# Optimization experiments

Hardware: AMD Instinct MI355X
Metric: run time of the kernel (lower is better)

## Reference

```python
import jax, jax.numpy as jnp
import numpy as np

K_HOPS = 10  # truncation order of the heat-kernel Taylor series


def setup_inputs() -> dict:
    key = jax.random.key(0)
    k1, k2, k3 = jax.random.split(key, 3)
    N, E, D_IN, D_OUT = 50000, 625000, 128, 128
    x = jax.random.normal(k1, (N, D_IN), dtype=jnp.float32)
    edge_index = jax.random.randint(k2, (2, E), 0, N, dtype=jnp.int64)
    t = jnp.asarray(5.0, dtype=jnp.float32)  # learnable diffusion time
    lim = 1.0 / np.sqrt(D_IN)
    W = jax.random.uniform(k3, (D_OUT, D_IN), dtype=jnp.float32, minval=-lim, maxval=lim)
    b = jnp.zeros((D_OUT,), dtype=jnp.float32)
    return {"x": x, "edge_index": edge_index, "t": t, "W": W, "b": b}


def reference(x, edge_index, t, W, b):
    N = x.shape[0]
    loop = jnp.arange(N, dtype=edge_index.dtype)
    src = jnp.concatenate([edge_index[0], loop])  # gcn_norm adds self-loops
    dst = jnp.concatenate([edge_index[1], loop])
    # symmetric normalization: norm_e = deg(dst)^-1/2 * deg(src)^-1/2
    deg = jnp.zeros((N,), dtype=x.dtype).at[dst].add(1.0)
    dinv = jnp.where(deg > 0, jax.lax.rsqrt(deg), 0.0)
    norm = dinv[src] * dinv[dst]  # [E+N]

    def prop(h):  # one hop of A_hat @ h via gather-scale-scatter
        msg = h[src] * norm[:, None]          # [E+N, D]
        return jax.ops.segment_sum(msg, dst, num_segments=N)

    # heat kernel: e^{-t} * sum_k t^k/k! * A_hat^k x
    coeff = jnp.exp(-t)
    out = coeff * x
    h = x
    for k in range(1, K_HOPS + 1):
        h = prop(h)
        coeff = coeff * t / k
        out = out + coeff * h
    return out @ W.T + b
```

## Files before the change

### kernel.cpp

```cpp
#include <hip/hip_runtime.h>
#include <math.h>

typedef float f4 __attribute__((ext_vector_type(4)));
typedef _Float16 h4 __attribute__((ext_vector_type(4)));


__global__ void k_count(const int* __restrict__ dst, int* __restrict__ cnt, int E) {
  int e = blockIdx.x * blockDim.x + threadIdx.x;
  if (e < E) atomicAdd(&cnt[dst[e]], 1);
}

__global__ void k_scan_partial(const int* __restrict__ cnt, int* __restrict__ rowptr,
                               int* __restrict__ bsums, float* __restrict__ dinv, int N) {
  __shared__ int s[1024];
  int tid = threadIdx.x;
  int idx = blockIdx.x * 1024 + tid;
  int v = (idx < N) ? cnt[idx] : 0;
  if (idx < N) dinv[idx] = rsqrtf((float)(v + 1));
  s[tid] = v;
  __syncthreads();
  for (int off = 1; off < 1024; off <<= 1) {
    int add = (tid >= off) ? s[tid - off] : 0;
    __syncthreads();
    s[tid] += add;
    __syncthreads();
  }
  if (idx <= N) rowptr[idx] = s[tid] - v;
  if (tid == 1023) bsums[blockIdx.x] = s[1023];
}

__global__ void k_scan_sums(int* __restrict__ bsums, int nb) {
  __shared__ int s[1024];
  int tid = threadIdx.x;
  int v = (tid < nb) ? bsums[tid] : 0;
  s[tid] = v;
  __syncthreads();
  for (int off = 1; off < 1024; off <<= 1) {
    int add = (tid >= off) ? s[tid - off] : 0;
    __syncthreads();
    s[tid] += add;
    __syncthreads();
  }
  if (tid < nb) bsums[tid] = s[tid] - v;
}

__global__ void k_add_offsets(int* __restrict__ rowptr, int* __restrict__ cursor,
                              const int* __restrict__ bsums, int N) {
  int idx = blockIdx.x * 1024 + threadIdx.x;
  if (idx <= N) {
    int v = rowptr[idx] + bsums[blockIdx.x];
    rowptr[idx] = v;
    if (idx < N) cursor[idx] = v;
  }
}

__global__ void k_scatter(const int* __restrict__ src, const int* __restrict__ dst,
                          const float* __restrict__ dinv, int* __restrict__ cursor,
                          int2* __restrict__ colw, int E) {
  int e = blockIdx.x * blockDim.x + threadIdx.x;
  if (e < E) {
    int s = src[e];
    int d = dst[e];
    int slot = atomicAdd(&cursor[d], 1);
    colw[slot] = make_int2(s, __float_as_int(dinv[s] * dinv[d]));
  }
}

__global__ void k_tohalf(const float* __restrict__ x, _Float16* __restrict__ xh, int total4) {
  int i = blockIdx.x * blockDim.x + threadIdx.x;
  if (i < total4) ((h4*)xh)[i] = __builtin_convertvector(((const f4*)x)[i], h4);
}

__global__ __launch_bounds__(256) void k_hop(
    const int* __restrict__ rowptr, const int2* __restrict__ colw,
    const float* __restrict__ dinv, const h4* __restrict__ xh,
    const h4* __restrict__ yin, h4* __restrict__ yout,
    const float* __restrict__ t_ptr, int j, int first, int N) {
  int wave = threadIdx.x >> 6;
  int lane = threadIdx.x & 63;
  int half = lane >> 5;
  int fl = lane & 31;
  int r = (blockIdx.x * 4 + wave) * 2 + half;
  if (r >= N) return;
  float t = t_ptr[0];
  float cj = expf(-t);
  for (int i = 1; i <= j; ++i) cj *= t / (float)i;
  float gs = first ? cj * t / (float)(j + 1) : 1.0f;

  auto G = [&](int idx) -> f4 {
    return __builtin_convertvector(yin[(size_t)idx * 32 + fl], f4);
  };

  f4 sA = {0,0,0,0}, sB = {0,0,0,0}, sC = {0,0,0,0}, sD = {0,0,0,0};
  int e = rowptr[r], end = rowptr[r + 1];
  for (; e + 3 < end; e += 4) {
    int2 c0 = colw[e], c1 = colw[e + 1], c2 = colw[e + 2], c3 = colw[e + 3];
    sA += __int_as_float(c0.y) * G(c0.x);
    sB += __int_as_float(c1.y) * G(c1.x);
    sC += __int_as_float(c2.y) * G(c2.x);
    sD += __int_as_float(c3.y) * G(c3.x);
  }
  for (; e < end; ++e) {
    int2 c0 = colw[e];
    sA += __int_as_float(c0.y) * G(c0.x);
  }
  f4 s = (sA + sB) + (sC + sD);
  float di = dinv[r];
  s += (di * di) * G(r);
  f4 xr = __builtin_convertvector(xh[(size_t)r * 32 + fl], f4);
  s = gs * s + cj * xr;
  yout[(size_t)r * 32 + fl] = __builtin_convertvector(s, h4);
}

__global__ __launch_bounds__(256) void k_matmul(
    const h4* __restrict__ y16, const float* __restrict__ W,
    const float* __restrict__ bias, float* __restrict__ out, int N) {
  __shared__ float aS[64 * 128];
  __shared__ float wS[64 * 128];
  int tid = threadIdx.x;
  int rbase = blockIdx.x * 64;
  int cbase = blockIdx.y * 64;

  {
    int kq = tid & 31, rr = tid >> 5;
#pragma unroll
    for (int p = 0; p < 8; ++p) {
      int r = p * 8 + rr;
      int gr = rbase + r; if (gr >= N) gr = N - 1;
      f4 va = __builtin_convertvector(y16[(size_t)gr * 32 + kq], f4);
      *(f4*)&aS[r * 128 + ((kq ^ (r & 7)) << 2)] = va;
      f4 vw = *(const f4*)&W[(size_t)(cbase + r) * 128 + kq * 4];
      *(f4*)&wS[r * 128 + ((kq ^ (r & 7)) << 2)] = vw;
    }
  }
  __syncthreads();

  int rg = tid & 15, cg = tid >> 4;
  int sa = rg & 7;
  float s[4][4];
#pragma unroll
  for (int i = 0; i < 4; ++i)
#pragma unroll
    for (int j = 0; j < 4; ++j) s[i][j] = 0.f;

#pragma unroll 4
  for (int kq = 0; kq < 32; ++kq) {
    f4 a4[4], w4[4];
#pragma unroll
    for (int i = 0; i < 4; ++i)
      a4[i] = *(const f4*)&aS[(rg + 16 * i) * 128 + ((kq ^ sa) << 2)];
#pragma unroll
    for (int j = 0; j < 4; ++j) {
      int c = 4 * cg + j;
      w4[j] = *(const f4*)&wS[c * 128 + ((kq ^ (c & 7)) << 2)];
    }
#pragma unroll
    for (int i = 0; i < 4; ++i)
#pragma unroll
      for (int j = 0; j < 4; ++j)
        s[i][j] += a4[i].x * w4[j].x + a4[i].y * w4[j].y +
                   a4[i].z * w4[j].z + a4[i].w * w4[j].w;
  }

  f4 bv = *(const f4*)&bias[cbase + 4 * cg];
#pragma unroll
  for (int i = 0; i < 4; ++i) {
    int r = rbase + rg + 16 * i;
    if (r < N) {
      f4 o;
      o.x = s[i][0] + bv.x; o.y = s[i][1] + bv.y;
      o.z = s[i][2] + bv.z; o.w = s[i][3] + bv.w;
      *(f4*)&out[(size_t)r * 128 + cbase + 4 * cg] = o;
    }
  }
}


extern "C" void kernel_launch(void* const* d_in, const int* in_sizes, int n_in,
                              void* d_out, int out_size, void* d_ws, size_t ws_size,
                              hipStream_t stream) {
  const float* x = (const float*)d_in[0];
  const int* ei = (const int*)d_in[1];
  const float* t = (const float*)d_in[2];
  const float* W = (const float*)d_in[3];
  const float* b = (const float*)d_in[4];
  int N = in_sizes[0] / 128;
  int E = in_sizes[1] / 2;
  const int* srcp = ei;
  const int* dstp = ei + E;
  float* out = (float*)d_out;

  char* ws = (char*)d_ws;
  size_t off = 0;
  auto alloc = [&](size_t bytes) -> void* {
    void* p = ws + off;
    off += (bytes + 255) & ~(size_t)255;
    return p;
  };
  h4*    yh0    = (h4*)alloc((size_t)N * 128 * 2);
  h4*    yh1    = (h4*)alloc((size_t)N * 128 * 2);
  h4*    xh     = (h4*)alloc((size_t)N * 128 * 2);
  int*   cnt    = (int*)alloc((size_t)N * 4);
  float* dinv   = (float*)alloc((size_t)N * 4);
  int*   rowptr = (int*)alloc((size_t)(N + 1) * 4);
  int*   cursor = (int*)alloc((size_t)N * 4);
  int*   bsums  = (int*)alloc(4096);
  int2*  colw   = (int2*)alloc((size_t)E * 8);
  (void)ws_size;

  int nb_scan = (N + 1 + 1023) / 1024;

  hipMemsetAsync(cnt, 0, (size_t)N * 4, stream);
  k_count<<<(E + 255) / 256, 256, 0, stream>>>(dstp, cnt, E);
  k_scan_partial<<<nb_scan, 1024, 0, stream>>>(cnt, rowptr, bsums, dinv, N);
  k_scan_sums<<<1, 1024, 0, stream>>>(bsums, nb_scan);
  k_add_offsets<<<nb_scan, 1024, 0, stream>>>(rowptr, cursor, bsums, N);
  k_scatter<<<(E + 255) / 256, 256, 0, stream>>>(srcp, dstp, dinv, cursor, colw, E);
  k_tohalf<<<(N * 32 + 255) / 256, 256, 0, stream>>>(x, (_Float16*)xh, N * 32);

  int nblk = (N + 7) / 8;
  const h4* yin = xh;
  h4* bufs[2] = {yh0, yh1};
  for (int m = 0; m < 10; ++m) {
    h4* yout = bufs[m & 1];
    k_hop<<<nblk, 256, 0, stream>>>(rowptr, colw, dinv, xh, yin, yout,
                                    t, 9 - m, (m == 0) ? 1 : 0, N);
    yin = yout;
  }

  dim3 mmg((N + 63) / 64, 2);
  k_matmul<<<mmg, 256, 0, stream>>>(yin, W, b, out, N);
}
```

Before: 493.6 us.

## Use 16-byte fp16 gathers in hops and MFMA split-precision final matmul

The hop kernel now gives each row 16 lanes that each load 8 halves (16 bytes), so one wave covers four rows instead of two and each gather uses wider memory transactions. The final projection moves from an FP32 scalar LDS tile matmul to MFMA 16x16x32 f16 instructions. W is split into hi and lo fp16 parts so the fp16 rounding error of the weights is mostly recovered. This should cut matmul time and hop gather overhead, at the cost of fp16 products on activations and uncoalesced scalar output stores.

```diff
diff --git a/kernel.cpp b/kernel.cpp
--- a/kernel.cpp
+++ b/kernel.cpp
@@ -2,7 +2,8 @@
 #include <math.h>
 
 typedef float f4 __attribute__((ext_vector_type(4)));
-typedef _Float16 h4 __attribute__((ext_vector_type(4)));
+typedef float f8 __attribute__((ext_vector_type(8)));
+typedef _Float16 h8 __attribute__((ext_vector_type(8)));
 
 
 __global__ void k_count(const int* __restrict__ dst, int* __restrict__ cnt, int E) {
@@ -66,32 +67,36 @@
   }
 }
 
-__global__ void k_tohalf(const float* __restrict__ x, _Float16* __restrict__ xh, int total4) {
+__global__ void k_tohalf(const float* __restrict__ x, _Float16* __restrict__ xh, int total8) {
   int i = blockIdx.x * blockDim.x + threadIdx.x;
-  if (i < total4) ((h4*)xh)[i] = __builtin_convertvector(((const f4*)x)[i], h4);
+  if (i < total8) {
+    f4 a = ((const f4*)x)[i * 2], b = ((const f4*)x)[i * 2 + 1];
+    f8 v = {a.x, a.y, a.z, a.w, b.x, b.y, b.z, b.w};
+    ((h8*)xh)[i] = __builtin_convertvector(v, h8);
+  }
 }
 
 __global__ __launch_bounds__(256) void k_hop(
     const int* __restrict__ rowptr, const int2* __restrict__ colw,
-    const float* __restrict__ dinv, const h4* __restrict__ xh,
-    const h4* __restrict__ yin, h4* __restrict__ yout,
+    const float* __restrict__ dinv, const h8* __restrict__ xh,
+    const h8* __restrict__ yin, h8* __restrict__ yout,
     const float* __restrict__ t_ptr, int j, int first, int N) {
   int wave = threadIdx.x >> 6;
   int lane = threadIdx.x & 63;
-  int half = lane >> 5;
-  int fl = lane & 31;
-  int r = (blockIdx.x * 4 + wave) * 2 + half;
+  int quarter = lane >> 4;
+  int fl = lane & 15;
+  int r = (blockIdx.x * 4 + wave) * 4 + quarter;
   if (r >= N) return;
   float t = t_ptr[0];
   float cj = expf(-t);
   for (int i = 1; i <= j; ++i) cj *= t / (float)i;
   float gs = first ? cj * t / (float)(j + 1) : 1.0f;
 
-  auto G = [&](int idx) -> f4 {
-    return __builtin_convertvector(yin[(size_t)idx * 32 + fl], f4);
+  auto G = [&](int idx) -> f8 {
+    return __builtin_convertvector(yin[(size_t)idx * 16 + fl], f8);
   };
 
-  f4 sA = {0,0,0,0}, sB = {0,0,0,0}, sC = {0,0,0,0}, sD = {0,0,0,0};
+  f8 sA = {0,0,0,0,0,0,0,0}, sB = sA, sC = sA, sD = sA;
   int e = rowptr[r], end = rowptr[r + 1];
   for (; e + 3 < end; e += 4) {
     int2 c0 = colw[e], c1 = colw[e + 1], c2 = colw[e + 2], c3 = colw[e + 3];
@@ -104,73 +109,80 @@
     int2 c0 = colw[e];
     sA += __int_as_float(c0.y) * G(c0.x);
   }
-  f4 s = (sA + sB) + (sC + sD);
+  f8 s = (sA + sB) + (sC + sD);
   float di = dinv[r];
   s += (di * di) * G(r);
-  f4 xr = __builtin_convertvector(xh[(size_t)r * 32 + fl], f4);
+  f8 xr = __builtin_convertvector(xh[(size_t)r * 16 + fl], f8);
   s = gs * s + cj * xr;
-  yout[(size_t)r * 32 + fl] = __builtin_convertvector(s, h4);
+  yout[(size_t)r * 16 + fl] = __builtin_convertvector(s, h8);
 }
 
 __global__ __launch_bounds__(256) void k_matmul(
-    const h4* __restrict__ y16, const float* __restrict__ W,
+    const h8* __restrict__ y16, const float* __restrict__ W,
     const float* __restrict__ bias, float* __restrict__ out, int N) {
-  __shared__ float aS[64 * 128];
-  __shared__ float wS[64 * 128];
+  __shared__ h8 whiS[128 * 16];
+  __shared__ h8 wloS[128 * 16];
   int tid = threadIdx.x;
-  int rbase = blockIdx.x * 64;
-  int cbase = blockIdx.y * 64;
-
-  {
-    int kq = tid & 31, rr = tid >> 5;
-#pragma unroll
-    for (int p = 0; p < 8; ++p) {
-      int r = p * 8 + rr;
-      int gr = rbase + r; if (gr >= N) gr = N - 1;
-      f4 va = __builtin_convertvector(y16[(size_t)gr * 32 + kq], f4);
-      *(f4*)&aS[r * 128 + ((kq ^ (r & 7)) << 2)] = va;
-      f4 vw = *(const f4*)&W[(size_t)(cbase + r) * 128 + kq * 4];
-      *(f4*)&wS[r * 128 + ((kq ^ (r & 7)) << 2)] = vw;
+  int rblk = blockIdx.x * 128;
+
+#pragma unroll
+  for (int it = 0; it < 8; ++it) {
+    int idx = it * 256 + tid;
+    int n = idx >> 4, g = idx & 15;
+    f4 a = *(const f4*)&W[(size_t)n * 128 + g * 8];
+    f4 b = *(const f4*)&W[(size_t)n * 128 + g * 8 + 4];
+    f8 w = {a.x, a.y, a.z, a.w, b.x, b.y, b.z, b.w};
+    h8 hi = __builtin_convertvector(w, h8);
+    f8 hir = __builtin_convertvector(hi, f8);
+    h8 lo = __builtin_convertvector(w - hir, h8);
+    int slot = n * 16 + (g ^ (n & 7));
+    whiS[slot] = hi;
+    wloS[slot] = lo;
+  }
+  __syncthreads();
+
+  int wave = tid >> 6, lane = tid & 63;
+  int q = lane >> 4, fl = lane & 15;
+  int rbase = rblk + wave * 32;
+
+  f4 acc[2][8];
+#pragma unroll
+  for (int rt = 0; rt < 2; ++rt)
+#pragma unroll
+    for (int nt = 0; nt < 8; ++nt) acc[rt][nt] = (f4){0.f, 0.f, 0.f, 0.f};
+
+#pragma unroll
+  for (int s = 0; s < 4; ++s) {
+    h8 aA, aB;
+    {
+      int r0 = rbase + fl;       if (r0 >= N) r0 = N - 1;
+      int r1 = rbase + 16 + fl;  if (r1 >= N) r1 = N - 1;
+      aA = y16[(size_t)r0 * 16 + s * 4 + q];
+      aB = y16[(size_t)r1 * 16 + s * 4 + q];
     }
-  }
-  __syncthreads();
-
-  int rg = tid & 15, cg = tid >> 4;
-  int sa = rg & 7;
-  float s[4][4];
-#pragma unroll
-  for (int i = 0; i < 4; ++i)
-#pragma unroll
-    for (int j = 0; j < 4; ++j) s[i][j] = 0.f;
-
-#pragma unroll 4
-  for (int kq = 0; kq < 32; ++kq) {
-    f4 a4[4], w4[4];
-#pragma unroll
-    for (int i = 0; i < 4; ++i)
-      a4[i] = *(const f4*)&aS[(rg + 16 * i) * 128 + ((kq ^ sa) << 2)];
-#pragma unroll
-    for (int j = 0; j < 4; ++j) {
-      int c = 4 * cg + j;
-      w4[j] = *(const f4*)&wS[c * 128 + ((kq ^ (c & 7)) << 2)];
+#pragma unroll
+    for (int nt = 0; nt < 8; ++nt) {
+      int n = nt * 16 + fl;
+      int slot = n * 16 + ((s * 4 + q) ^ (n & 7));
+      h8 bh = whiS[slot];
+      h8 bl = wloS[slot];
+      acc[0][nt] = __builtin_amdgcn_mfma_f32_16x16x32_f16(aA, bh, acc[0][nt], 0, 0, 0);
+      acc[0][nt] = __builtin_amdgcn_mfma_f32_16x16x32_f16(aA, bl, acc[0][nt], 0, 0, 0);
+      acc[1][nt] = __builtin_amdgcn_mfma_f32_16x16x32_f16(aB, bh, acc[1][nt], 0, 0, 0);
+      acc[1][nt] = __builtin_amdgcn_mfma_f32_16x16x32_f16(aB, bl, acc[1][nt], 0, 0, 0);
     }
-#pragma unroll
-    for (int i = 0; i < 4; ++i)
-#pragma unroll
-      for (int j = 0; j < 4; ++j)
-        s[i][j] += a4[i].x * w4[j].x + a4[i].y * w4[j].y +
-                   a4[i].z * w4[j].z + a4[i].w * w4[j].w;
-  }
-
-  f4 bv = *(const f4*)&bias[cbase + 4 * cg];
-#pragma unroll
-  for (int i = 0; i < 4; ++i) {
-    int r = rbase + rg + 16 * i;
-    if (r < N) {
-      f4 o;
-      o.x = s[i][0] + bv.x; o.y = s[i][1] + bv.y;
-      o.z = s[i][2] + bv.z; o.w = s[i][3] + bv.w;
-      *(f4*)&out[(size_t)r * 128 + cbase + 4 * cg] = o;
+  }
+
+#pragma unroll
+  for (int rt = 0; rt < 2; ++rt) {
+#pragma unroll
+    for (int nt = 0; nt < 8; ++nt) {
+      float bv = bias[nt * 16 + fl];
+#pragma unroll
+      for (int reg = 0; reg < 4; ++reg) {
+        int r = rbase + rt * 16 + q * 4 + reg;
+        if (r < N) out[(size_t)r * 128 + nt * 16 + fl] = acc[rt][nt][reg] + bv;
+      }
     }
   }
 }
@@ -197,9 +209,9 @@
     off += (bytes + 255) & ~(size_t)255;
     return p;
   };
-  h4*    yh0    = (h4*)alloc((size_t)N * 128 * 2);
-  h4*    yh1    = (h4*)alloc((size_t)N * 128 * 2);
-  h4*    xh     = (h4*)alloc((size_t)N * 128 * 2);
+  h8*    yh0    = (h8*)alloc((size_t)N * 128 * 2);
+  h8*    yh1    = (h8*)alloc((size_t)N * 128 * 2);
+  h8*    xh     = (h8*)alloc((size_t)N * 128 * 2);
   int*   cnt    = (int*)alloc((size_t)N * 4);
   float* dinv   = (float*)alloc((size_t)N * 4);
   int*   rowptr = (int*)alloc((size_t)(N + 1) * 4);
@@ -216,18 +228,17 @@
   k_scan_sums<<<1, 1024, 0, stream>>>(bsums, nb_scan);
   k_add_offsets<<<nb_scan, 1024, 0, stream>>>(rowptr, cursor, bsums, N);
   k_scatter<<<(E + 255) / 256, 256, 0, stream>>>(srcp, dstp, dinv, cursor, colw, E);
-  k_tohalf<<<(N * 32 + 255) / 256, 256, 0, stream>>>(x, (_Float16*)xh, N * 32);
-
-  int nblk = (N + 7) / 8;
-  const h4* yin = xh;
-  h4* bufs[2] = {yh0, yh1};
+  k_tohalf<<<(N * 16 + 255) / 256, 256, 0, stream>>>(x, (_Float16*)xh, N * 16);
+
+  int nblk = (N + 15) / 16;
+  const h8* yin = xh;
+  h8* bufs[2] = {yh0, yh1};
   for (int m = 0; m < 10; ++m) {
-    h4* yout = bufs[m & 1];
+    h8* yout = bufs[m & 1];
     k_hop<<<nblk, 256, 0, stream>>>(rowptr, colw, dinv, xh, yin, yout,
                                     t, 9 - m, (m == 0) ? 1 : 0, N);
     yin = yout;
   }
 
-  dim3 mmg((N + 63) / 64, 2);
-  k_matmul<<<mmg, 256, 0, stream>>>(yin, W, b, out, N);
-}
+  k_matmul<<<(N + 127) / 128, 256, 0, stream>>>(yin, W, b, out, N);
+}
```

Measured after the change: 458.0 us. -7.2%, faster.
